# Kernel optimization log

Measured on AMD Instinct MI355X. Metric: run time of the kernel, lower is better.

## Reference

```python
import jax, jax.numpy as jnp
import numpy as np

WS = 8          # window_size
NH = 8          # num_heads
VD = 512        # values_dim
CD = 128        # coords_dim
INNER = 512     # inner_ratio * values_dim
E = INNER // NH # head_dim = 64
B, Hh, Ww_ = 2, 224, 224

# relative position indices (static)
_idx = np.array([[x, y] for x in range(WS) for y in range(WS)])
_rel = _idx[None, :, :] - _idx[:, None, :] + WS - 1  # (WS^2, WS^2, 2)
REL0 = jnp.asarray(_rel[:, :, 0])
REL1 = jnp.asarray(_rel[:, :, 1])

# shifted-window masks (static)
_s = WS * (WS // 2)
_rm = np.zeros((WS * WS, WS * WS), np.float32)
_rm[-_s:, :-_s] = -np.inf
_rm[:-_s, -_s:] = -np.inf
_cm = _rm.reshape(WS, WS, WS, WS).transpose(1, 0, 3, 2).reshape(WS * WS, WS * WS)
ROW_MASK = jnp.asarray(_rm)
COL_MASK = jnp.asarray(_cm)


def _rmsnorm(x, g, eps=1e-6):
    return x * g * jax.lax.rsqrt(jnp.mean(x * x, axis=-1, keepdims=True) + eps)


def _to_windows(x, b, Wh, Ww):
    # x: (b, hp, wp, INNER) with channel layout (e H) (head fastest)
    x = x.reshape(b, Wh, WS, Ww, WS, E, NH)
    return x.transpose(0, 6, 1, 3, 2, 4, 5).reshape(b, NH, Wh, Ww, WS * WS, E)


def setup_inputs() -> dict:
    key = jax.random.key(0)
    ks = jax.random.split(key, 8)
    s = 0.02
    return {
        "embedded_values": jax.random.normal(ks[0], (B, Hh, Ww_, VD), jnp.float32),
        "embedded_coords": jax.random.normal(ks[1], (B, Hh, Ww_, CD), jnp.float32),
        "Wqk_v": jax.random.normal(ks[2], (VD, 2 * INNER), jnp.float32) * s,
        "bqk_v": jnp.zeros((2 * INNER,), jnp.float32),
        "g_v": jnp.ones((2 * INNER,), jnp.float32),
        "Wv": jax.random.normal(ks[3], (VD, INNER), jnp.float32) * s,
        "bv": jnp.zeros((INNER,), jnp.float32),
        "Wqk_c": jax.random.normal(ks[4], (CD, 2 * INNER), jnp.float32) * s,
        "bqk_c": jnp.zeros((2 * INNER,), jnp.float32),
        "g_c": jnp.ones((2 * INNER,), jnp.float32),
        "pos_emb": jax.random.normal(ks[5], (2 * WS - 1, 2 * WS - 1), jnp.float32),
        "Wout": jax.random.normal(ks[6], (INNER, VD), jnp.float32) * s,
        "bout": jnp.zeros((VD,), jnp.float32),
    }


def reference(embedded_values, embedded_coords, Wqk_v, bqk_v, g_v, Wv, bv,
              Wqk_c, bqk_c, g_c, pos_emb, Wout, bout):
    b, h, w, _ = embedded_values.shape
    # projections; torch concat then rearrange '(d k)' k=3 interleaves channels -> reshape (..., INNER, 3)
    vqk = _rmsnorm(embedded_values @ Wqk_v + bqk_v, g_v)          # (b,h,w,2*INNER)
    vval = embedded_values @ Wv + bv                               # (b,h,w,INNER)
    v = jnp.concatenate([vqk, vval], axis=-1).reshape(b, h, w, INNER, 3)
    c = _rmsnorm(embedded_coords @ Wqk_c + bqk_c, g_c).reshape(b, h, w, INNER, 2)

    pad_h = (-h) % WS
    pad_w = (-w) % WS
    v = jnp.pad(v, ((0, 0), (0, pad_h), (0, pad_w), (0, 0), (0, 0)))
    c = jnp.pad(c, ((0, 0), (0, pad_h), (0, pad_w), (0, 0), (0, 0)))
    # shifted=True: roll windows by half window (no inverse roll in original)
    v = jnp.roll(v, (-(WS // 2), -(WS // 2)), axis=(1, 2))
    c = jnp.roll(c, (-(WS // 2), -(WS // 2)), axis=(1, 2))

    hp, wp = h + pad_h, w + pad_w
    Wh, Ww = hp // WS, wp // WS
    qv = _to_windows(v[..., 0], b, Wh, Ww)
    kv = _to_windows(v[..., 1], b, Wh, Ww)
    vv = _to_windows(v[..., 2], b, Wh, Ww)
    qc = _to_windows(c[..., 0], b, Wh, Ww)
    kc = _to_windows(c[..., 1], b, Wh, Ww)

    scale = float(E) ** 0.5
    dots = (jnp.einsum('bhijpe,bhijqe->bhijpq', qv, kv)
            + jnp.einsum('bhijpe,bhijqe->bhijpq', qc, kc)) / scale
    dots = dots + pos_emb[REL0, REL1]
    # shifted-window masks on last window row / column
    dots = dots.at[:, :, -1, :].add(ROW_MASK)
    dots = dots.at[:, :, :, -1].add(COL_MASK)

    attn = jax.nn.softmax(dots, axis=-1)
    y = jnp.einsum('bhijpq,bhijqe->bhijpe', attn, vv)
    # un-window; output channel layout is (H e) (head slow)
    y = y.reshape(b, NH, Wh, Ww, WS, WS, E).transpose(0, 2, 4, 3, 5, 1, 6)
    y = y.reshape(b, hp, wp, INNER)[:, :h, :w, :]
    return y @ Wout + bout
```

## Files before the change

### kernel.cpp

```cpp
#include <hip/hip_runtime.h>


using u16 = unsigned short;
typedef short bf16x8 __attribute__((ext_vector_type(8)));
typedef float f32x4 __attribute__((ext_vector_type(4)));
typedef u16 u16x4 __attribute__((ext_vector_type(4)));
typedef u16 u16x8 __attribute__((ext_vector_type(8)));

__device__ __forceinline__ float bf2f(u16 v) {
  return __uint_as_float(((unsigned)v) << 16);
}
__device__ __forceinline__ u16 f2bf(float f) {
  unsigned u = __float_as_uint(f);
  u += 0x7fffu + ((u >> 16) & 1u);
  return (u16)(u >> 16);
}

__device__ __forceinline__ void gld16(const u16* g, u16* l) {
  __builtin_amdgcn_global_load_lds(
      (const __attribute__((address_space(1))) unsigned*)g,
      (__attribute__((address_space(3))) unsigned*)l, 16, 0, 0);
}

struct f8 { float v[8]; };
__device__ __forceinline__ f8 ld8(const float* p) {
  f8 r;
  *(float4*)&r.v[0] = *(const float4*)p;
  *(float4*)&r.v[4] = *(const float4*)(p + 4);
  return r;
}
__device__ __forceinline__ bf16x8 nfrag(u16x8 raw, const f8& A, const f8& B, float s) {
  u16x8 o;
#pragma unroll
  for (int j = 0; j < 8; ++j) o[j] = f2bf(bf2f(raw[j]) * (A.v[j] * s + B.v[j]));
  return *(bf16x8*)&o;
}
__device__ __forceinline__ bf16x8 nfragA(u16x8 raw, const f8& A, float s) {
  u16x8 o;
#pragma unroll
  for (int j = 0; j < 8; ++j) o[j] = f2bf(bf2f(raw[j]) * (A.v[j] * s));
  return *(bf16x8*)&o;
}

__global__ void conv_bf16(const float* __restrict__ in, u16* __restrict__ out) {
  size_t i = ((size_t)blockIdx.x * 256 + threadIdx.x) * 8;
  float4 a = *(const float4*)(in + i);
  float4 b = *(const float4*)(in + i + 4);
  u16x8 o;
  o[0] = f2bf(a.x); o[1] = f2bf(a.y); o[2] = f2bf(a.z); o[3] = f2bf(a.w);
  o[4] = f2bf(b.x); o[5] = f2bf(b.y); o[6] = f2bf(b.z); o[7] = f2bf(b.w);
  *(u16x8*)(out + i) = o;
}

__global__ void prep_wv(const float* __restrict__ Wqkv, const float* __restrict__ Wv,
                        u16* __restrict__ out) {
  int idx = blockIdx.x * 256 + threadIdx.x;
  if (idx >= 1536 * 512) return;
  int j = idx >> 9, kk = idx & 511;
  int t = j >> 9, rr = j & 511, nn = rr >> 6, e = rr & 63;
  int cc = 3 * (e * 8 + nn) + t;
  float v = (cc < 1024) ? Wqkv[kk * 1024 + cc] : Wv[kk * 512 + (cc - 1024)];
  out[idx] = f2bf(v);
}

__global__ void prep_wc(const float* __restrict__ W, u16* __restrict__ out) {
  int idx = blockIdx.x * 256 + threadIdx.x;
  if (idx >= 1024 * 128) return;
  int j = idx >> 7, kk = idx & 127;
  int t = j >> 9, rr = j & 511, nn = rr >> 6, e = rr & 63;
  int cc = 2 * (e * 8 + nn) + t;
  out[idx] = f2bf(W[kk * 1024 + cc]);
}

__global__ void prep_wout(const float* __restrict__ W, u16* __restrict__ out) {
  int idx = blockIdx.x * 256 + threadIdx.x;
  if (idx >= 512 * 512) return;
  int o = idx >> 9, kk = idx & 511;
  out[idx] = f2bf(W[kk * 512 + o]);
}

__global__ void prep_vec(const float* __restrict__ bqkv, const float* __restrict__ g_v,
                         const float* __restrict__ bv, const float* __restrict__ bqkc,
                         const float* __restrict__ g_c,
                         float* __restrict__ bpv, float* __restrict__ gAv, float* __restrict__ gBv,
                         float* __restrict__ bpc, float* __restrict__ gAc, float* __restrict__ gBc) {
  int j = blockIdx.x * 256 + threadIdx.x;
  if (j < 1536) {
    int t = j >> 9, rr = j & 511, nn = rr >> 6, e = rr & 63;
    int cc = 3 * (e * 8 + nn) + t;
    if (cc < 1024) { bpv[j] = bqkv[cc]; gAv[j] = g_v[cc]; gBv[j] = 0.f; }
    else           { bpv[j] = bv[cc - 1024]; gAv[j] = 0.f; gBv[j] = 1.f; }
  }
  if (j < 1024) {
    int t = j >> 9, rr = j & 511, nn = rr >> 6, e = rr & 63;
    int cc = 2 * (e * 8 + nn) + t;
    bpc[j] = bqkc[cc]; gAc[j] = g_c[cc]; gBc[j] = 0.f;
  }
}

__global__ void prep_biasT(const float* __restrict__ pe, float* __restrict__ bT) {
  int idx = blockIdx.x * 256 + threadIdx.x;
  if (idx >= 4 * 4096) return;
  int v = idx >> 12, q = (idx >> 6) & 63, p = idx & 63;
  int ap = p >> 3, bp = p & 7, aq = q >> 3, bq = q & 7;
  float val = pe[(aq - ap + 7) * 15 + (bq - bp + 7)];
  if ((v & 1) && ((ap >= 4) != (aq >= 4))) val = -1e30f;
  if ((v & 2) && ((bp >= 4) != (bq >= 4))) val = -1e30f;
  bT[idx] = val;
}

template<int N, int K, int MODE>
__global__ __launch_bounds__(256) void gemm_bt(
    const u16* __restrict__ A, const u16* __restrict__ Bt,
    const float* __restrict__ bias, void* __restrict__ outp,
    float* __restrict__ part, const float* __restrict__ gB, int nwg) {
  constexpr int NCB = N / 128;
  constexpr int KT = K / 64;
  const int orig = blockIdx.x;
  const int work = (orig & 7) * (nwg >> 3) + (orig >> 3);
  const int bm = work / NCB, bn = work % NCB;

  const int tid = threadIdx.x;
  const int w = tid >> 6;
  const int lane = tid & 63;
  const int wr = w >> 1, wc = w & 1;
  const int g = lane >> 4, c = lane & 15;

  __shared__ u16 As[128 * 64];
  __shared__ u16 Bs[128 * 64];

  f32x4 acc[4][4] = {};
  const u16* Ag = A + (size_t)bm * 128 * K;
  const u16* Bg = Bt + (size_t)bn * 128 * K;

  auto stage = [&](int kt) {
    const int k0 = kt * 64;
#pragma unroll
    for (int i = 0; i < 4; ++i) {
      const int idx = i * 256 + tid;
      const int row = idx >> 3, p = idx & 7;
      const int q = p ^ (row & 7);
      gld16(Ag + (size_t)row * K + k0 + q * 8, As + idx * 8);
      gld16(Bg + (size_t)row * K + k0 + q * 8, Bs + idx * 8);
    }
  };

  const int cm = c & 7;
  for (int kt = 0; kt < KT; ++kt) {
    stage(kt);
    __syncthreads();
#pragma unroll
    for (int kk = 0; kk < 2; ++kk) {
      bf16x8 af[4], bfv[4];
#pragma unroll
      for (int mi = 0; mi < 4; ++mi)
        af[mi] = *(const bf16x8*)(As + (wr * 64 + mi * 16 + c) * 64 +
                                  ((4 * kk + g) ^ cm) * 8);
#pragma unroll
      for (int ni = 0; ni < 4; ++ni)
        bfv[ni] = *(const bf16x8*)(Bs + (wc * 64 + ni * 16 + c) * 64 +
                                   ((4 * kk + g) ^ cm) * 8);
#pragma unroll
      for (int mi = 0; mi < 4; ++mi)
#pragma unroll
        for (int ni = 0; ni < 4; ++ni)
          acc[mi][ni] = __builtin_amdgcn_mfma_f32_16x16x32_bf16(bfv[ni], af[mi], acc[mi][ni], 0, 0, 0);
    }
    __syncthreads();
  }

  const int rowbase = bm * 128 + wr * 64;
  const int colbase = bn * 128 + wc * 64;
  if constexpr (MODE == 0) {
    u16* O = (u16*)outp;
    float rowsq[4] = {0.f, 0.f, 0.f, 0.f};
#pragma unroll
    for (int ni = 0; ni < 4; ++ni) {
      const int col4 = colbase + ni * 16 + g * 4;
      const float4 bb = *(const float4*)(bias + col4);
      const float4 gb = *(const float4*)(gB + col4);
#pragma unroll
      for (int mi = 0; mi < 4; ++mi) {
        const int row = rowbase + mi * 16 + c;
        u16x4 pk;
        float v0 = acc[mi][ni][0] + bb.x;
        float v1 = acc[mi][ni][1] + bb.y;
        float v2 = acc[mi][ni][2] + bb.z;
        float v3 = acc[mi][ni][3] + bb.w;
        pk[0] = f2bf(v0); pk[1] = f2bf(v1); pk[2] = f2bf(v2); pk[3] = f2bf(v3);
        *(u16x4*)(O + (size_t)row * N + col4) = pk;
        rowsq[mi] += (gb.x == 0.f ? v0 * v0 : 0.f) + (gb.y == 0.f ? v1 * v1 : 0.f)
                   + (gb.z == 0.f ? v2 * v2 : 0.f) + (gb.w == 0.f ? v3 * v3 : 0.f);
      }
    }
#pragma unroll
    for (int mi = 0; mi < 4; ++mi) {
      float s = rowsq[mi];
      s += __shfl_xor(s, 16);
      s += __shfl_xor(s, 32);
      rowsq[mi] = s;
    }
    float* red = (float*)As;
    if (g == 0) {
#pragma unroll
      for (int mi = 0; mi < 4; ++mi)
        red[wc * 128 + wr * 64 + mi * 16 + c] = rowsq[mi];
    }
    __syncthreads();
    if (tid < 128)
      part[(size_t)(bm * 128 + tid) * NCB + bn] = red[tid] + red[128 + tid];
  } else {
    float* O = (float*)outp;
#pragma unroll
    for (int ni = 0; ni < 4; ++ni) {
      const int col4 = colbase + ni * 16 + g * 4;
      const float4 bb = *(const float4*)(bias + col4);
#pragma unroll
      for (int mi = 0; mi < 4; ++mi) {
        const int row = rowbase + mi * 16 + c;
        f32x4 o;
        o[0] = acc[mi][ni][0] + bb.x;
        o[1] = acc[mi][ni][1] + bb.y;
        o[2] = acc[mi][ni][2] + bb.z;
        o[3] = acc[mi][ni][3] + bb.w;
        *(f32x4*)(O + (size_t)row * N + col4) = o;
      }
    }
  }
}

__global__ void combine_scales(const float* __restrict__ pvp, const float* __restrict__ pcp,
                               float* __restrict__ sv, float* __restrict__ sc) {
  const int i = blockIdx.x * 256 + threadIdx.x;
  float s = 0.f;
#pragma unroll
  for (int k = 0; k < 12; ++k) s += pvp[(size_t)i * 12 + k];
  sv[i] = rsqrtf(s * (1.f / 1024.f) + 1e-6f);
  float s2 = 0.f;
#pragma unroll
  for (int k = 0; k < 8; ++k) s2 += pcp[(size_t)i * 8 + k];
  sc[i] = rsqrtf(s2 * (1.f / 1024.f) + 1e-6f);
}

__global__ __launch_bounds__(64) void attn_kernel(
    const u16* __restrict__ Pv, const u16* __restrict__ Pc,
    const float* __restrict__ sv, const float* __restrict__ sc,
    const float* __restrict__ gAv, const float* __restrict__ gBv,
    const float* __restrict__ gAc, const float* __restrict__ gBc,
    const float* __restrict__ biasT, u16* __restrict__ Y) {
  const int l = threadIdx.x;
  int bx = blockIdx.x;
  const int wj = bx % 28; bx /= 28;
  const int wi = bx % 28; bx /= 28;
  const int n = bx & 7;
  const int bi = bx >> 3;

  const int g = l >> 4, c = l & 15;
  const int rr0 = l >> 3, rch = l & 7;

  __shared__ u16 Vl[64 * 72];
  __shared__ u16 Pl[64 * 72];

  auto pixof = [&](int a, int b2) -> int {
    int y = wi * 8 + a + 4; if (y >= 224) y -= 224;
    int x = wj * 8 + b2 + 4; if (x >= 224) x -= 224;
    return (bi * 224 + y) * 224 + x;
  };

  int pixr[4]; float svr[4], scr[4];
#pragma unroll
  for (int r = 0; r < 4; ++r) {
    const int p = r * 16 + c;
    pixr[r] = pixof(p >> 3, p & 7);
    svr[r] = sv[pixr[r]];
    scr[r] = sc[pixr[r]];
  }

  u16x8 vreg[8]; float vs_[8];
#pragma unroll
  for (int i = 0; i < 8; ++i) {
    const int pix = pixof(i, rr0);
    vs_[i] = sv[pix];
    vreg[i] = *(const u16x8*)(Pv + (size_t)pix * 1536 + 1024 + n * 64 + rch * 8);
  }

  f32x4 acc[4][4] = {};
#pragma unroll
  for (int kk = 0; kk < 2; ++kk) {
    const int e0 = kk * 32 + g * 8;
    const f8 qA = ld8(gAv + n * 64 + e0), qB = ld8(gBv + n * 64 + e0);
    const f8 kA = ld8(gAv + 512 + n * 64 + e0), kB = ld8(gBv + 512 + n * 64 + e0);
    bf16x8 af[4], bq[4];
#pragma unroll
    for (int r = 0; r < 4; ++r) {
      const u16* src = Pv + (size_t)pixr[r] * 1536 + n * 64 + e0;
      af[r] = nfrag(*(const u16x8*)(src + 512), kA, kB, svr[r]);
      bq[r] = nfrag(*(const u16x8*)src, qA, qB, svr[r]);
    }
#pragma unroll
    for (int mi = 0; mi < 4; ++mi)
#pragma unroll
      for (int ni = 0; ni < 4; ++ni)
        acc[mi][ni] = __builtin_amdgcn_mfma_f32_16x16x32_bf16(af[mi], bq[ni], acc[mi][ni], 0, 0, 0);
  }
#pragma unroll
  for (int kk = 0; kk < 2; ++kk) {
    const int e0 = kk * 32 + g * 8;
    const f8 qA = ld8(gAc + n * 64 + e0);
    const f8 kA = ld8(gAc + 512 + n * 64 + e0);
    bf16x8 af[4], bq[4];
#pragma unroll
    for (int r = 0; r < 4; ++r) {
      const u16* src = Pc + (size_t)pixr[r] * 1024 + n * 64 + e0;
      af[r] = nfragA(*(const u16x8*)(src + 512), kA, scr[r]);
      bq[r] = nfragA(*(const u16x8*)src, qA, scr[r]);
    }
#pragma unroll
    for (int mi = 0; mi < 4; ++mi)
#pragma unroll
      for (int ni = 0; ni < 4; ++ni)
        acc[mi][ni] = __builtin_amdgcn_mfma_f32_16x16x32_bf16(af[mi], bq[ni], acc[mi][ni], 0, 0, 0);
  }

  const int variant = ((wi == 27) ? 1 : 0) | ((wj == 27) ? 2 : 0);
  const float* BT = biasT + variant * 4096;
#pragma unroll
  for (int mi = 0; mi < 4; ++mi)
#pragma unroll
    for (int ni = 0; ni < 4; ++ni)
#pragma unroll
      for (int r = 0; r < 4; ++r) {
        const int q = mi * 16 + g * 4 + r;
        const int p = ni * 16 + c;
        acc[mi][ni][r] = acc[mi][ni][r] * 0.125f + BT[q * 64 + p];
      }
  float rinv[4];
#pragma unroll
  for (int ni = 0; ni < 4; ++ni) {
    float m = -3.0e38f;
#pragma unroll
    for (int mi = 0; mi < 4; ++mi)
#pragma unroll
      for (int r = 0; r < 4; ++r) m = fmaxf(m, acc[mi][ni][r]);
    m = fmaxf(m, __shfl_xor(m, 16));
    m = fmaxf(m, __shfl_xor(m, 32));
    float ssum = 0.f;
#pragma unroll
    for (int mi = 0; mi < 4; ++mi)
#pragma unroll
      for (int r = 0; r < 4; ++r) {
        float e = __expf(acc[mi][ni][r] - m);
        acc[mi][ni][r] = e;
        ssum += e;
      }
    ssum += __shfl_xor(ssum, 16);
    ssum += __shfl_xor(ssum, 32);
    rinv[ni] = 1.f / ssum;
  }

#pragma unroll
  for (int mi = 0; mi < 4; ++mi)
#pragma unroll
    for (int ni = 0; ni < 4; ++ni) {
      u16x4 pk;
#pragma unroll
      for (int r = 0; r < 4; ++r) pk[r] = f2bf(acc[mi][ni][r] * rinv[ni]);
      *(u16x4*)(Pl + (ni * 16 + c) * 72 + mi * 16 + g * 4) = pk;
    }
  {
    const f8 vA = ld8(gAv + 1024 + n * 64 + rch * 8);
    const f8 vB = ld8(gBv + 1024 + n * 64 + rch * 8);
#pragma unroll
    for (int i = 0; i < 8; ++i) {
      bf16x8 nv = nfrag(vreg[i], vA, vB, vs_[i]);
      *(bf16x8*)(Vl + (i * 8 + rr0) * 72 + rch * 8) = nv;
    }
  }

  f32x4 ya[4][4] = {};
#pragma unroll
  for (int kk = 0; kk < 2; ++kk) {
    bf16x8 pa[4];
#pragma unroll
    for (int mi = 0; mi < 4; ++mi)
      pa[mi] = *(const bf16x8*)(Pl + (mi * 16 + c) * 72 + kk * 32 + g * 8);
#pragma unroll
    for (int ni = 0; ni < 4; ++ni) {
      u16x8 vtmp;
#pragma unroll
      for (int j = 0; j < 8; ++j)
        vtmp[j] = Vl[(kk * 32 + g * 8 + j) * 72 + ni * 16 + c];
      bf16x8 vb = *(bf16x8*)&vtmp;
#pragma unroll
      for (int mi = 0; mi < 4; ++mi)
        ya[mi][ni] = __builtin_amdgcn_mfma_f32_16x16x32_bf16(pa[mi], vb, ya[mi][ni], 0, 0, 0);
    }
  }

  u16* Yt = Pl;
#pragma unroll
  for (int mi = 0; mi < 4; ++mi)
#pragma unroll
    for (int ni = 0; ni < 4; ++ni) {
      u16x4 yk;
#pragma unroll
      for (int r = 0; r < 4; ++r) yk[r] = f2bf(ya[mi][ni][r]);
      *(u16x4*)(Yt + (ni * 16 + c) * 72 + mi * 16 + g * 4) = yk;
    }
#pragma unroll
  for (int it = 0; it < 8; ++it) {
    const int b2 = l >> 3;
    const int ch = l & 7;
    const int p = it * 8 + b2;
    u16x8 row;
#pragma unroll
    for (int j = 0; j < 8; ++j) row[j] = Yt[(ch * 8 + j) * 72 + p];
    const int oy = wi * 8 + it, ox = wj * 8 + b2;
    *(u16x8*)(Y + ((size_t)(bi * 224 + oy) * 224 + ox) * 512 + n * 64 + ch * 8) = row;
  }
}

extern "C" void kernel_launch(void* const* d_in, const int* in_sizes, int n_in,
                              void* d_out, int out_size, void* d_ws, size_t ws_size,
                              hipStream_t stream) {
  const float* ev   = (const float*)d_in[0];
  const float* ec   = (const float*)d_in[1];
  const float* Wqkv = (const float*)d_in[2];
  const float* bqkv = (const float*)d_in[3];
  const float* g_v  = (const float*)d_in[4];
  const float* Wv   = (const float*)d_in[5];
  const float* bv   = (const float*)d_in[6];
  const float* Wqkc = (const float*)d_in[7];
  const float* bqkc = (const float*)d_in[8];
  const float* g_c  = (const float*)d_in[9];
  const float* pe   = (const float*)d_in[10];
  const float* Wout = (const float*)d_in[11];
  const float* bout = (const float*)d_in[12];
  float* out = (float*)d_out;

  char* w = (char*)d_ws;
  auto take = [&](size_t b) { char* p = w; w += (b + 255) & ~(size_t)255; return p; };
  u16* Wvp   = (u16*)take(1536ull * 512 * 2);
  u16* Wcp   = (u16*)take(1024ull * 128 * 2);
  u16* Wob   = (u16*)take(512ull * 512 * 2);
  float* bpv = (float*)take(1536 * 4);
  float* gAv = (float*)take(1536 * 4);
  float* gBv = (float*)take(1536 * 4);
  float* bpc = (float*)take(1024 * 4);
  float* gAc = (float*)take(1024 * 4);
  float* gBc = (float*)take(1024 * 4);
  float* bT  = (float*)take(4 * 4096 * 4);
  u16* Pv    = (u16*)take(100352ull * 1536 * 2);
  u16* Pc    = (u16*)take(100352ull * 1024 * 2);
  float* pvp = (float*)take(100352ull * 12 * 4);
  float* pcp = (float*)take(100352ull * 8 * 4);
  float* sv  = (float*)take(100352ull * 4);
  float* sc  = (float*)take(100352ull * 4);
  u16* Yb    = (u16*)take(100352ull * 512 * 2);
  u16* evb   = Yb;
  u16* ecb   = (u16*)take(100352ull * 128 * 2);

  conv_bf16<<<25088, 256, 0, stream>>>(ev, evb);
  conv_bf16<<<6272, 256, 0, stream>>>(ec, ecb);
  prep_wv<<<3072, 256, 0, stream>>>(Wqkv, Wv, Wvp);
  prep_wc<<<512, 256, 0, stream>>>(Wqkc, Wcp);
  prep_wout<<<1024, 256, 0, stream>>>(Wout, Wob);
  prep_vec<<<6, 256, 0, stream>>>(bqkv, g_v, bv, bqkc, g_c, bpv, gAv, gBv, bpc, gAc, gBc);
  prep_biasT<<<64, 256, 0, stream>>>(pe, bT);

  gemm_bt<1536, 512, 0><<<9408, 256, 0, stream>>>(evb, Wvp, bpv, Pv, pvp, gBv, 9408);
  gemm_bt<1024, 128, 0><<<6272, 256, 0, stream>>>(ecb, Wcp, bpc, Pc, pcp, gBc, 6272);
  combine_scales<<<392, 256, 0, stream>>>(pvp, pcp, sv, sc);
  attn_kernel<<<12544, 64, 0, stream>>>(Pv, Pc, sv, sc, gAv, gBv, gAc, gBc, bT, Yb);
  gemm_bt<512, 512, 1><<<3136, 256, 0, stream>>>(Yb, Wob, bout, out, nullptr, nullptr, 3136);
}
```

Baseline: 739.5 us.

## Double-buffer K=512 GEMMs and pass softmax probabilities via shuffles in attention

The K=512 GEMMs switch to a double-buffered 32-wide K tile with a new swizzle and a 4-blocks-per-SM launch bound, so the next tile's global-to-LDS load overlaps the current tile's MFMAs. The K=128 GEMM keeps the old single-buffer kernel. In the attention kernel, the softmax probabilities are no longer written to a shared-memory buffer. They are rearranged into MFMA A-operand layout with cross-lane shuffles, which removes one LDS buffer and its round trip. The trade-off is more barriers per K (twice as many K steps) and extra shuffle/select instructions.

```diff
diff --git a/kernel.cpp b/kernel.cpp
--- a/kernel.cpp
+++ b/kernel.cpp
@@ -6,6 +6,7 @@
 typedef float f32x4 __attribute__((ext_vector_type(4)));
 typedef u16 u16x4 __attribute__((ext_vector_type(4)));
 typedef u16 u16x8 __attribute__((ext_vector_type(8)));
+typedef unsigned u32x4 __attribute__((ext_vector_type(4)));
 
 __device__ __forceinline__ float bf2f(u16 v) {
   return __uint_as_float(((unsigned)v) << 16);
@@ -110,12 +111,12 @@
 }
 
 template<int N, int K, int MODE>
-__global__ __launch_bounds__(256) void gemm_bt(
+__global__ __launch_bounds__(256, 4) void gemm_db(
     const u16* __restrict__ A, const u16* __restrict__ Bt,
     const float* __restrict__ bias, void* __restrict__ outp,
     float* __restrict__ part, const float* __restrict__ gB, int nwg) {
   constexpr int NCB = N / 128;
-  constexpr int KT = K / 64;
+  constexpr int KT = K / 32;
   const int orig = blockIdx.x;
   const int work = (orig & 7) * (nwg >> 3) + (orig >> 3);
   const int bm = work / NCB, bn = work % NCB;
@@ -126,46 +127,45 @@
   const int wr = w >> 1, wc = w & 1;
   const int g = lane >> 4, c = lane & 15;
 
-  __shared__ u16 As[128 * 64];
-  __shared__ u16 Bs[128 * 64];
+  __shared__ u16 As[2 * 4096];
+  __shared__ u16 Bs[2 * 4096];
 
   f32x4 acc[4][4] = {};
   const u16* Ag = A + (size_t)bm * 128 * K;
   const u16* Bg = Bt + (size_t)bn * 128 * K;
 
-  auto stage = [&](int kt) {
-    const int k0 = kt * 64;
-#pragma unroll
-    for (int i = 0; i < 4; ++i) {
+  auto stage = [&](int buf, int kt) {
+    const int k0 = kt * 32;
+#pragma unroll
+    for (int i = 0; i < 2; ++i) {
       const int idx = i * 256 + tid;
-      const int row = idx >> 3, p = idx & 7;
-      const int q = p ^ (row & 7);
-      gld16(Ag + (size_t)row * K + k0 + q * 8, As + idx * 8);
-      gld16(Bg + (size_t)row * K + k0 + q * 8, Bs + idx * 8);
+      const int row = idx >> 2, ch = idx & 3;
+      const int sch = ch ^ ((row >> 1) & 3);
+      gld16(Ag + (size_t)row * K + k0 + sch * 8, As + buf * 4096 + idx * 8);
+      gld16(Bg + (size_t)row * K + k0 + sch * 8, Bs + buf * 4096 + idx * 8);
     }
   };
 
-  const int cm = c & 7;
+  stage(0, 0);
+  __syncthreads();
+
+  const int swz = (c >> 1) & 3;
   for (int kt = 0; kt < KT; ++kt) {
-    stage(kt);
-    __syncthreads();
-#pragma unroll
-    for (int kk = 0; kk < 2; ++kk) {
-      bf16x8 af[4], bfv[4];
-#pragma unroll
-      for (int mi = 0; mi < 4; ++mi)
-        af[mi] = *(const bf16x8*)(As + (wr * 64 + mi * 16 + c) * 64 +
-                                  ((4 * kk + g) ^ cm) * 8);
+    if (kt + 1 < KT) stage((kt + 1) & 1, kt + 1);
+    const u16* Ab = As + (kt & 1) * 4096;
+    const u16* Bb = Bs + (kt & 1) * 4096;
+    bf16x8 af[4], bfv[4];
+#pragma unroll
+    for (int mi = 0; mi < 4; ++mi)
+      af[mi] = *(const bf16x8*)(Ab + (wr * 64 + mi * 16 + c) * 32 + (g ^ swz) * 8);
+#pragma unroll
+    for (int ni = 0; ni < 4; ++ni)
+      bfv[ni] = *(const bf16x8*)(Bb + (wc * 64 + ni * 16 + c) * 32 + (g ^ swz) * 8);
+#pragma unroll
+    for (int mi = 0; mi < 4; ++mi)
 #pragma unroll
       for (int ni = 0; ni < 4; ++ni)
-        bfv[ni] = *(const bf16x8*)(Bs + (wc * 64 + ni * 16 + c) * 64 +
-                                   ((4 * kk + g) ^ cm) * 8);
-#pragma unroll
-      for (int mi = 0; mi < 4; ++mi)
-#pragma unroll
-        for (int ni = 0; ni < 4; ++ni)
-          acc[mi][ni] = __builtin_amdgcn_mfma_f32_16x16x32_bf16(bfv[ni], af[mi], acc[mi][ni], 0, 0, 0);
-    }
+        acc[mi][ni] = __builtin_amdgcn_mfma_f32_16x16x32_bf16(bfv[ni], af[mi], acc[mi][ni], 0, 0, 0);
     __syncthreads();
   }
 
@@ -229,6 +229,126 @@
   }
 }
 
+template<int N, int K, int MODE>
+__global__ __launch_bounds__(256) void gemm_sb(
+    const u16* __restrict__ A, const u16* __restrict__ Bt,
+    const float* __restrict__ bias, void* __restrict__ outp,
+    float* __restrict__ part, const float* __restrict__ gB, int nwg) {
+  constexpr int NCB = N / 128;
+  constexpr int KT = K / 64;
+  const int orig = blockIdx.x;
+  const int work = (orig & 7) * (nwg >> 3) + (orig >> 3);
+  const int bm = work / NCB, bn = work % NCB;
+
+  const int tid = threadIdx.x;
+  const int w = tid >> 6;
+  const int lane = tid & 63;
+  const int wr = w >> 1, wc = w & 1;
+  const int g = lane >> 4, c = lane & 15;
+
+  __shared__ u16 As[128 * 64];
+  __shared__ u16 Bs[128 * 64];
+
+  f32x4 acc[4][4] = {};
+  const u16* Ag = A + (size_t)bm * 128 * K;
+  const u16* Bg = Bt + (size_t)bn * 128 * K;
+
+  auto stage = [&](int kt) {
+    const int k0 = kt * 64;
+#pragma unroll
+    for (int i = 0; i < 4; ++i) {
+      const int idx = i * 256 + tid;
+      const int row = idx >> 3, p = idx & 7;
+      const int q = p ^ (row & 7);
+      gld16(Ag + (size_t)row * K + k0 + q * 8, As + idx * 8);
+      gld16(Bg + (size_t)row * K + k0 + q * 8, Bs + idx * 8);
+    }
+  };
+
+  const int cm = c & 7;
+  for (int kt = 0; kt < KT; ++kt) {
+    stage(kt);
+    __syncthreads();
+#pragma unroll
+    for (int kk = 0; kk < 2; ++kk) {
+      bf16x8 af[4], bfv[4];
+#pragma unroll
+      for (int mi = 0; mi < 4; ++mi)
+        af[mi] = *(const bf16x8*)(As + (wr * 64 + mi * 16 + c) * 64 +
+                                  ((4 * kk + g) ^ cm) * 8);
+#pragma unroll
+      for (int ni = 0; ni < 4; ++ni)
+        bfv[ni] = *(const bf16x8*)(Bs + (wc * 64 + ni * 16 + c) * 64 +
+                                   ((4 * kk + g) ^ cm) * 8);
+#pragma unroll
+      for (int mi = 0; mi < 4; ++mi)
+#pragma unroll
+        for (int ni = 0; ni < 4; ++ni)
+          acc[mi][ni] = __builtin_amdgcn_mfma_f32_16x16x32_bf16(bfv[ni], af[mi], acc[mi][ni], 0, 0, 0);
+    }
+    __syncthreads();
+  }
+
+  const int rowbase = bm * 128 + wr * 64;
+  const int colbase = bn * 128 + wc * 64;
+  if constexpr (MODE == 0) {
+    u16* O = (u16*)outp;
+    float rowsq[4] = {0.f, 0.f, 0.f, 0.f};
+#pragma unroll
+    for (int ni = 0; ni < 4; ++ni) {
+      const int col4 = colbase + ni * 16 + g * 4;
+      const float4 bb = *(const float4*)(bias + col4);
+      const float4 gb = *(const float4*)(gB + col4);
+#pragma unroll
+      for (int mi = 0; mi < 4; ++mi) {
+        const int row = rowbase + mi * 16 + c;
+        u16x4 pk;
+        float v0 = acc[mi][ni][0] + bb.x;
+        float v1 = acc[mi][ni][1] + bb.y;
+        float v2 = acc[mi][ni][2] + bb.z;
+        float v3 = acc[mi][ni][3] + bb.w;
+        pk[0] = f2bf(v0); pk[1] = f2bf(v1); pk[2] = f2bf(v2); pk[3] = f2bf(v3);
+        *(u16x4*)(O + (size_t)row * N + col4) = pk;
+        rowsq[mi] += (gb.x == 0.f ? v0 * v0 : 0.f) + (gb.y == 0.f ? v1 * v1 : 0.f)
+                   + (gb.z == 0.f ? v2 * v2 : 0.f) + (gb.w == 0.f ? v3 * v3 : 0.f);
+      }
+    }
+#pragma unroll
+    for (int mi = 0; mi < 4; ++mi) {
+      float s = rowsq[mi];
+      s += __shfl_xor(s, 16);
+      s += __shfl_xor(s, 32);
+      rowsq[mi] = s;
+    }
+    float* red = (float*)As;
+    if (g == 0) {
+#pragma unroll
+      for (int mi = 0; mi < 4; ++mi)
+        red[wc * 128 + wr * 64 + mi * 16 + c] = rowsq[mi];
+    }
+    __syncthreads();
+    if (tid < 128)
+      part[(size_t)(bm * 128 + tid) * NCB + bn] = red[tid] + red[128 + tid];
+  } else {
+    float* O = (float*)outp;
+#pragma unroll
+    for (int ni = 0; ni < 4; ++ni) {
+      const int col4 = colbase + ni * 16 + g * 4;
+      const float4 bb = *(const float4*)(bias + col4);
+#pragma unroll
+      for (int mi = 0; mi < 4; ++mi) {
+        const int row = rowbase + mi * 16 + c;
+        f32x4 o;
+        o[0] = acc[mi][ni][0] + bb.x;
+        o[1] = acc[mi][ni][1] + bb.y;
+        o[2] = acc[mi][ni][2] + bb.z;
+        o[3] = acc[mi][ni][3] + bb.w;
+        *(f32x4*)(O + (size_t)row * N + col4) = o;
+      }
+    }
+  }
+}
+
 __global__ void combine_scales(const float* __restrict__ pvp, const float* __restrict__ pcp,
                                float* __restrict__ sv, float* __restrict__ sc) {
   const int i = blockIdx.x * 256 + threadIdx.x;
@@ -259,7 +379,6 @@
   const int rr0 = l >> 3, rch = l & 7;
 
   __shared__ u16 Vl[64 * 72];
-  __shared__ u16 Pl[64 * 72];
 
   auto pixof = [&](int a, int b2) -> int {
     int y = wi * 8 + a + 4; if (y >= 224) y -= 224;
@@ -358,32 +477,49 @@
     rinv[ni] = 1.f / ssum;
   }
 
-#pragma unroll
-  for (int mi = 0; mi < 4; ++mi)
-#pragma unroll
-    for (int ni = 0; ni < 4; ++ni) {
-      u16x4 pk;
-#pragma unroll
-      for (int r = 0; r < 4; ++r) pk[r] = f2bf(acc[mi][ni][r] * rinv[ni]);
-      *(u16x4*)(Pl + (ni * 16 + c) * 72 + mi * 16 + g * 4) = pk;
-    }
   {
     const f8 vA = ld8(gAv + 1024 + n * 64 + rch * 8);
     const f8 vB = ld8(gBv + 1024 + n * 64 + rch * 8);
 #pragma unroll
-    for (int i = 0; i < 8; ++i) {
-      bf16x8 nv = nfrag(vreg[i], vA, vB, vs_[i]);
-      *(bf16x8*)(Vl + (i * 8 + rr0) * 72 + rch * 8) = nv;
+    for (int i = 0; i < 8; ++i)
+      *(bf16x8*)(Vl + (i * 8 + rr0) * 72 + rch * 8) = nfrag(vreg[i], vA, vB, vs_[i]);
+  }
+
+  const int L0 = ((l & 16) << 1) + c;
+  const int L1 = L0 + 16;
+  const bool hiA = (l >> 5) & 1;
+  bf16x8 pa2[2][4];
+#pragma unroll
+  for (int mi = 0; mi < 4; ++mi) {
+    unsigned pk[4][2];
+#pragma unroll
+    for (int a = 0; a < 4; ++a)
+#pragma unroll
+      for (int b = 0; b < 2; ++b)
+        pk[a][b] = (unsigned)f2bf(acc[a][mi][2 * b] * rinv[mi]) |
+                   ((unsigned)f2bf(acc[a][mi][2 * b + 1] * rinv[mi]) << 16);
+#pragma unroll
+    for (int kk = 0; kk < 2; ++kk) {
+      unsigned ca = (unsigned)__shfl((int)pk[2 * kk][0], L0);
+      unsigned da = (unsigned)__shfl((int)pk[2 * kk + 1][0], L0);
+      unsigned cb = (unsigned)__shfl((int)pk[2 * kk][1], L0);
+      unsigned db_ = (unsigned)__shfl((int)pk[2 * kk + 1][1], L0);
+      unsigned cc2 = (unsigned)__shfl((int)pk[2 * kk][0], L1);
+      unsigned dc = (unsigned)__shfl((int)pk[2 * kk + 1][0], L1);
+      unsigned cd = (unsigned)__shfl((int)pk[2 * kk][1], L1);
+      unsigned dd = (unsigned)__shfl((int)pk[2 * kk + 1][1], L1);
+      u32x4 t;
+      t[0] = hiA ? da : ca;
+      t[1] = hiA ? db_ : cb;
+      t[2] = hiA ? dc : cc2;
+      t[3] = hiA ? dd : cd;
+      pa2[kk][mi] = *(bf16x8*)&t;
     }
   }
 
   f32x4 ya[4][4] = {};
 #pragma unroll
   for (int kk = 0; kk < 2; ++kk) {
-    bf16x8 pa[4];
-#pragma unroll
-    for (int mi = 0; mi < 4; ++mi)
-      pa[mi] = *(const bf16x8*)(Pl + (mi * 16 + c) * 72 + kk * 32 + g * 8);
 #pragma unroll
     for (int ni = 0; ni < 4; ++ni) {
       u16x8 vtmp;
@@ -393,11 +529,11 @@
       bf16x8 vb = *(bf16x8*)&vtmp;
 #pragma unroll
       for (int mi = 0; mi < 4; ++mi)
-        ya[mi][ni] = __builtin_amdgcn_mfma_f32_16x16x32_bf16(pa[mi], vb, ya[mi][ni], 0, 0, 0);
-    }
-  }
-
-  u16* Yt = Pl;
+        ya[mi][ni] = __builtin_amdgcn_mfma_f32_16x16x32_bf16(pa2[kk][mi], vb, ya[mi][ni], 0, 0, 0);
+    }
+  }
+
+  u16* Yt = Vl;
 #pragma unroll
   for (int mi = 0; mi < 4; ++mi)
 #pragma unroll
@@ -468,9 +604,9 @@
   prep_vec<<<6, 256, 0, stream>>>(bqkv, g_v, bv, bqkc, g_c, bpv, gAv, gBv, bpc, gAc, gBc);
   prep_biasT<<<64, 256, 0, stream>>>(pe, bT);
 
-  gemm_bt<1536, 512, 0><<<9408, 256, 0, stream>>>(evb, Wvp, bpv, Pv, pvp, gBv, 9408);
-  gemm_bt<1024, 128, 0><<<6272, 256, 0, stream>>>(ecb, Wcp, bpc, Pc, pcp, gBc, 6272);
+  gemm_db<1536, 512, 0><<<9408, 256, 0, stream>>>(evb, Wvp, bpv, Pv, pvp, gBv, 9408);
+  gemm_sb<1024, 128, 0><<<6272, 256, 0, stream>>>(ecb, Wcp, bpc, Pc, pcp, gBc, 6272);
   combine_scales<<<392, 256, 0, stream>>>(pvp, pcp, sv, sc);
   attn_kernel<<<12544, 64, 0, stream>>>(Pv, Pc, sv, sc, gAv, gBv, gAc, gBc, bT, Yb);
-  gemm_bt<512, 512, 1><<<3136, 256, 0, stream>>>(Yb, Wob, bout, out, nullptr, nullptr, 3136);
-}
+  gemm_db<512, 512, 1><<<3136, 256, 0, stream>>>(Yb, Wob, bout, out, nullptr, nullptr, 3136);
+}
```

Result: slower. 785.3 us (+6.2%).
